# Performance work log

Hardware: AMD Instinct MI355X
Metric: run time of the kernel (lower is better)

Reference implementation:

```python
import jax, jax.numpy as jnp
import numpy as np

B, S, H = 4, 4096, 256
NH, W = 8, 128
DH = H // NH
FF = 1024
NEG = -1e9

def gelu(x):
    return jax.nn.gelu(x, approximate=False)

def layer_norm(x, g, b, eps=1e-9):
    # torch .std() is unbiased (ddof=1); note the (std + eps) denominator, not sqrt(var+eps)
    mean = jnp.mean(x, axis=-1, keepdims=True)
    std = jnp.std(x, axis=-1, keepdims=True, ddof=1)
    return g * (x - mean) / (std + eps) + b

def causal_conv(x, w, b, dilation):
    # x: (B,S,C), w: (9, Cin, Cout); left-padded causal conv (Conv class)
    pad = dilation * 8
    y = jax.lax.conv_general_dilated(x, w, window_strides=(1,), padding=[(pad, 0)],
                                     rhs_dilation=(dilation,), dimension_numbers=('NWC', 'WIO', 'NWC'))
    return y + b

def sliding_window_attention(q, k, v, bias):
    # q,k,v: (B,NH,S,DH); q pre-scaled. Faithful to Longformer sliding_chunks_matmul_qk/pv:
    # band of 2W+1 relative offsets per query, out-of-range keys masked to -inf before softmax.
    b, h, s, d = q.shape
    c = s // W  # number of length-W query chunks
    qc = q.reshape(b, h, c, W, d)
    kp = jnp.pad(k, ((0, 0), (0, 0), (W, W), (0, 0)))
    vp = jnp.pad(v, ((0, 0), (0, 0), (W, W), (0, 0)))
    kidx = (jnp.arange(c) * W)[:, None] + jnp.arange(3 * W)[None, :]  # (c,3W) overlapping key chunks
    kc = kp[:, :, kidx, :]  # (b,h,c,3W,d)
    vc = vp[:, :, kidx, :]
    scores = jnp.einsum('bhcxd,bhcyd->bhcxy', qc, kc)  # (b,h,c,W,3W)
    x = jnp.arange(W)
    r = jnp.arange(2 * W + 1)
    band_idx = x[:, None] + r[None, :]  # (W,2W+1), values in [0,3W-1]
    band = jnp.take_along_axis(scores, band_idx[None, None, None], axis=-1)  # (b,h,c,W,2W+1)
    i = jnp.arange(s).reshape(c, W)
    j = i[:, :, None] + (r - W)[None, None, :]  # global key index per band entry
    valid = (j >= 0) & (j < s)
    band = jnp.where(valid[None, None], band + bias, NEG)  # relative bias depends only on offset
    probs = jax.nn.softmax(band.astype(jnp.float32), axis=-1).astype(q.dtype)
    ridx = jnp.arange(3 * W)[None, :] - x[:, None]  # (W,3W) inverse band->chunk map
    vmask = ((ridx >= 0) & (ridx <= 2 * W)).astype(probs.dtype)
    pc = jnp.take_along_axis(probs, jnp.clip(ridx, 0, 2 * W)[None, None, None], axis=-1) * vmask[None, None, None]
    return jnp.einsum('bhcxy,bhcyd->bhcxd', pc, vc).reshape(b, h, s, d)


def setup_inputs() -> dict:
    key = jax.random.key(0)
    ks = jax.random.split(key, 12)
    inputs = jax.random.normal(ks[0], (B, S, H), jnp.float32)
    dw_w = jax.random.normal(ks[1], (9,), jnp.float32) * 0.1   # depthwise (9,1) kernel, 1 channel
    dw_b = jnp.zeros((1,), jnp.float32)
    pw_w = jax.random.normal(ks[2], (3,), jnp.float32) * 0.5   # pointwise 1->3 conv (scalars)
    pw_b = jnp.zeros((3,), jnp.float32)
    Wq = jax.random.normal(ks[3], (H, H), jnp.float32) * 0.02
    Wk = jax.random.normal(ks[4], (H, H), jnp.float32) * 0.02
    Wv = jax.random.normal(ks[5], (H, H), jnp.float32) * 0.02
    Wo = jax.random.normal(ks[6], (H, H), jnp.float32) * 0.02
    rel_bias = jax.random.normal(ks[7], (2 * S,), jnp.float32) * 0.02
    ln1_g = jnp.ones((H,), jnp.float32); ln1_b = jnp.zeros((H,), jnp.float32)
    ln2_g = jnp.ones((H,), jnp.float32); ln2_b = jnp.zeros((H,), jnp.float32)
    w1 = jax.random.normal(ks[8], (9, H, FF), jnp.float32) * 0.02
    b1 = jnp.zeros((FF,), jnp.float32)
    w2 = jax.random.normal(ks[9], (9, FF, H), jnp.float32) * 0.02
    b2 = jnp.zeros((H,), jnp.float32)
    return {"inputs": inputs, "dw_w": dw_w, "dw_b": dw_b, "pw_w": pw_w, "pw_b": pw_b,
            "Wq": Wq, "Wk": Wk, "Wv": Wv, "Wo": Wo, "rel_bias": rel_bias,
            "ln1_g": ln1_g, "ln1_b": ln1_b, "ln2_g": ln2_g, "ln2_b": ln2_b,
            "w1": w1, "b1": b1, "w2": w2, "b2": b2}


def reference(inputs, dw_w, dw_b, pw_w, pw_b, Wq, Wk, Wv, Wo, rel_bias,
              ln1_g, ln1_b, ln2_g, ln2_b, w1, b1, w2, b2):
    x = inputs
    xn = layer_norm(x, ln1_g, ln1_b)
    # SepConv2d QKV generator: depthwise (9,1) conv along seq (shared over features), GELU,
    # pointwise 1x1 conv 1->3 channels, then GELU again (self.relu in MHA.forward)
    xp = jnp.pad(xn, ((0, 0), (4, 4), (0, 0)))
    dw = jnp.zeros_like(xn)
    for t in range(9):
        dw = dw + dw_w[t] * xp[:, t:t + S, :]
    dw = dw + dw_b[0]
    hmid = gelu(dw)
    qkv = gelu(hmid[None] * pw_w.reshape(3, 1, 1, 1) + pw_b.reshape(3, 1, 1, 1))  # (3,B,S,H)
    q = qkv[0] @ Wq
    k = qkv[1] @ Wk
    v = qkv[2] @ Wv
    split = lambda t: t.reshape(B, S, NH, DH).transpose(0, 2, 1, 3)
    q, k, v = split(q), split(k), split(v)
    q = q * (DH ** -0.5)
    # relative_position_index = arange(2W+1).repeat(lens,1) -> bias uses table[:2W+1] per offset
    bias = rel_bias[:2 * W + 1]
    ctx = sliding_window_attention(q, k, v, bias)
    ctx = ctx.transpose(0, 2, 1, 3).reshape(B, S, H)
    x = x + ctx @ Wo
    xn2 = layer_norm(x, ln2_g, ln2_b)
    # PositionwiseFeedForward 'cc': causal dilated convs; GELU applied after every layer (incl. last)
    f = gelu(causal_conv(xn2, w1, b1, 1))
    f = gelu(causal_conv(f, w2, b2, 8))
    return x + f
```

## Files before the change

### kernel.cpp

```cpp
#include <hip/hip_runtime.h>
#include <stdint.h>

typedef uint16_t u16;
typedef uint32_t u32;

typedef __attribute__((ext_vector_type(8))) short bf16x8;
typedef __attribute__((ext_vector_type(4))) float f32x4;

typedef __attribute__((address_space(1))) const u32 gas_u32;
typedef __attribute__((address_space(3))) u32 las_u32;

#define S_LEN 4096
#define HDIM  256
#define FFDIM 1024

__device__ __forceinline__ float bf2f(u16 u) { return __uint_as_float(((u32)u) << 16); }
__device__ __forceinline__ u16 f2bf(float f) {
  u32 x = __float_as_uint(f);
  return (u16)((x + 0x7fffu + ((x >> 16) & 1u)) >> 16);
}
__device__ __forceinline__ float gelu_f(float x) {
  return 0.5f * x * (1.0f + erff(x * 0.7071067811865475f));
}
__device__ __forceinline__ void glds16(const u16* g, u16* l) {
  __builtin_amdgcn_global_load_lds((gas_u32*)g, (las_u32*)l, 16, 0, 0);
}

__global__ __launch_bounds__(256) void ktranspose_all(
    const float* __restrict__ Wq, const float* __restrict__ Wk, const float* __restrict__ Wv,
    const float* __restrict__ Wo, const float* __restrict__ W1, const float* __restrict__ W2,
    u16* __restrict__ WqT, u16* __restrict__ WkT, u16* __restrict__ WvT,
    u16* __restrict__ WoT, u16* __restrict__ W1T, u16* __restrict__ W2T, float qscale) {
  __shared__ u16 t[32][33];
  const int bid = blockIdx.x;
  const float* in; u16* out; int K, N; float scale = 1.0f; int idx;
  if (bid < 256) {
    K = 256; N = 256; idx = bid & 63;
    const int w = bid >> 6;
    in = (w == 0) ? Wq : (w == 1) ? Wk : (w == 2) ? Wv : Wo;
    out = (w == 0) ? WqT : (w == 1) ? WkT : (w == 2) ? WvT : WoT;
    if (w == 0) scale = qscale;
  } else if (bid < 2560) {
    K = 2304; N = 1024; idx = bid - 256; in = W1; out = W1T;
  } else {
    K = 9216; N = 256; idx = bid - 2560; in = W2; out = W2T;
  }
  const int kt = K >> 5;
  const int k0 = (idx % kt) * 32, n0 = (idx / kt) * 32;
  const int tx = threadIdx.x, ty = threadIdx.y;
#pragma unroll
  for (int i = ty; i < 32; i += 8) t[i][tx] = f2bf(in[(long)(k0 + i) * N + (n0 + tx)] * scale);
  __syncthreads();
#pragma unroll
  for (int i = ty; i < 32; i += 8) out[(long)(n0 + i) * K + (k0 + tx)] = t[tx][i];
}

template <int OUTBF>
__global__ __launch_bounds__(256) void ln_kernel(const float* __restrict__ inv, void* __restrict__ outv,
                                                 const float* __restrict__ g, const float* __restrict__ bsh,
                                                 int OSEGR, int OGUARD,
                                                 uint4* __restrict__ gx, uint4* __restrict__ gf) {
  const int tid = threadIdx.x;
  if (OUTBF && blockIdx.x >= 4096) {
    int t = (blockIdx.x - 4096) * 256 + tid;
    const uint4 z = {0u, 0u, 0u, 0u};
    if (t < 1024) {
      const int s = t >> 8, o = t & 255;
      gx[(long)s * 131328 + o] = z;
    } else {
      t -= 1024;
      if (t < 32768) {
        const int s = t >> 13, o = t & 8191;
        gf[(long)s * 532480 + o] = z;
      }
    }
    return;
  }
  const int lane = tid & 63;
  const long row = (long)blockIdx.x * 4 + (tid >> 6);
  const int c0 = lane * 4;
  float v[4];
  float4 f = *(const float4*)(inv + row * HDIM + c0);
  v[0] = f.x; v[1] = f.y; v[2] = f.z; v[3] = f.w;
  float s = v[0] + v[1] + v[2] + v[3];
#pragma unroll
  for (int o = 32; o > 0; o >>= 1) s += __shfl_xor(s, o);
  const float mean = s * (1.0f / 256.0f);
  float ss = 0.f;
#pragma unroll
  for (int j = 0; j < 4; ++j) { float d = v[j] - mean; ss += d * d; }
#pragma unroll
  for (int o = 32; o > 0; o >>= 1) ss += __shfl_xor(ss, o);
  const float inv_ = 1.0f / (sqrtf(ss * (1.0f / 255.0f)) + 1e-9f);
  float y[4];
#pragma unroll
  for (int j = 0; j < 4; ++j) y[j] = g[c0 + j] * (v[j] - mean) * inv_ + bsh[c0 + j];
  if (OUTBF) {
    const long orow = (row >> 12) * OSEGR + OGUARD + (row & (S_LEN - 1));
    uint2 o_;
    o_.x = (u32)f2bf(y[0]) | ((u32)f2bf(y[1]) << 16);
    o_.y = (u32)f2bf(y[2]) | ((u32)f2bf(y[3]) << 16);
    *(uint2*)((u16*)outv + orow * HDIM + c0) = o_;
  } else {
    float4 o_; o_.x = y[0]; o_.y = y[1]; o_.z = y[2]; o_.w = y[3];
    *(float4*)((float*)outv + row * HDIM + c0) = o_;
  }
}

__global__ __launch_bounds__(256) void dwconv_qkv(const float* __restrict__ xn,
                                                  u16* __restrict__ gq, u16* __restrict__ gk, u16* __restrict__ gv,
                                                  const float* __restrict__ dw_w, const float* __restrict__ dw_b,
                                                  const float* __restrict__ pw_w, const float* __restrict__ pw_b) {
  const int tid = threadIdx.x;
  const int lane = tid & 63;
  const long row = (long)blockIdx.x * 4 + (tid >> 6);
  const int sl = (int)(row & (S_LEN - 1));
  const float b0 = dw_b[0];
  float a0 = b0, a1 = b0, a2 = b0, a3 = b0;
#pragma unroll
  for (int t = 0; t < 9; ++t) {
    const int s2 = sl + t - 4;
    if (s2 >= 0 && s2 < S_LEN) {
      const float w = dw_w[t];
      float4 xv = *(const float4*)(xn + (row + t - 4) * HDIM + lane * 4);
      a0 = fmaf(w, xv.x, a0); a1 = fmaf(w, xv.y, a1);
      a2 = fmaf(w, xv.z, a2); a3 = fmaf(w, xv.w, a3);
    }
  }
  float h[4];
  h[0] = gelu_f(a0); h[1] = gelu_f(a1); h[2] = gelu_f(a2); h[3] = gelu_f(a3);
  u16* outs[3] = {gq, gk, gv};
#pragma unroll
  for (int p = 0; p < 3; ++p) {
    const float pw = pw_w[p], pb = pw_b[p];
    float y[4];
#pragma unroll
    for (int j = 0; j < 4; ++j) y[j] = gelu_f(fmaf(h[j], pw, pb));
    uint2 o_;
    o_.x = (u32)f2bf(y[0]) | ((u32)f2bf(y[1]) << 16);
    o_.y = (u32)f2bf(y[2]) | ((u32)f2bf(y[3]) << 16);
    *(uint2*)(outs[p] + row * HDIM + lane * 4) = o_;
  }
}

__global__ __launch_bounds__(256) void gemm_big(
    const u16* __restrict__ A, const u16* __restrict__ BT, void* __restrict__ Outv,
    u16* __restrict__ vt, int KW, int N, long a_z, long b_z, long o_z) {
  __shared__ __align__(16) u16 As[256 * 64];
  __shared__ __align__(16) u16 Bs[128 * 64];
  const int tid = threadIdx.x;
  const int lane = tid & 63;
  const int wid = tid >> 6;
  const int wm = (wid & 1) * 128;
  const int wn = (wid >> 1) * 64;
  const int fm = lane & 15;
  const int fq = lane >> 4;
  const int t0 = blockIdx.x * 256;
  const int n0 = blockIdx.y * 128;
  A += (long)blockIdx.z * a_z;
  BT += (long)blockIdx.z * b_z;

  const int srow = lane >> 3;
  const int cseg = (((lane & 7) ^ srow) << 3);

  f32x4 acc[8][4];
#pragma unroll
  for (int a = 0; a < 8; ++a)
#pragma unroll
    for (int b = 0; b < 4; ++b) acc[a][b] = (f32x4){0.f, 0.f, 0.f, 0.f};

  for (int k0 = 0; k0 < KW; k0 += 64) {
    for (int op = wid; op < 32; op += 4)
      glds16(A + (long)(t0 + op * 8 + srow) * KW + k0 + cseg, &As[op * 8 * 64]);
#pragma unroll
    for (int j = 0; j < 4; ++j)
      glds16(BT + (long)(n0 + wid * 32 + j * 8 + srow) * KW + k0 + cseg,
             &Bs[(wid * 32 + j * 8) * 64]);
    __syncthreads();
#pragma unroll
    for (int kk = 0; kk < 2; ++kk) {
      const int g = kk * 4 + fq;
      bf16x8 af[8], bfv[4];
#pragma unroll
      for (int t = 0; t < 8; ++t) {
        const int ra = wm + t * 16 + fm;
        af[t] = *(const bf16x8*)&As[ra * 64 + ((g ^ (ra & 7)) << 3)];
      }
#pragma unroll
      for (int t = 0; t < 4; ++t) {
        const int rb = wn + t * 16 + fm;
        bfv[t] = *(const bf16x8*)&Bs[rb * 64 + ((g ^ (rb & 7)) << 3)];
      }
#pragma unroll
      for (int mi = 0; mi < 8; ++mi)
#pragma unroll
        for (int ni = 0; ni < 4; ++ni)
          acc[mi][ni] = __builtin_amdgcn_mfma_f32_16x16x32_bf16(af[mi], bfv[ni], acc[mi][ni], 0, 0, 0);
    }
    __syncthreads();
  }

#pragma unroll
  for (int mi = 0; mi < 8; ++mi)
#pragma unroll
    for (int ni = 0; ni < 4; ++ni) {
      if (blockIdx.z == 2) {
        const int col = n0 + wn + ni * 16 + fm;
        const int hh = col >> 5, dd = col & 31;
        const long trow0 = t0 + wm + mi * 16 + fq * 4;
        const long bb = trow0 >> 12;
        const int s0 = (int)(trow0 & (S_LEN - 1));
        uint2 o_;
        o_.x = (u32)f2bf(acc[mi][ni][0]) | ((u32)f2bf(acc[mi][ni][1]) << 16);
        o_.y = (u32)f2bf(acc[mi][ni][2]) | ((u32)f2bf(acc[mi][ni][3]) << 16);
        *(uint2*)(vt + ((bb * 8 + hh) * 32 + dd) * S_LEN + s0) = o_;
      } else {
#pragma unroll
        for (int r = 0; r < 4; ++r) {
          const long trow = t0 + wm + mi * 16 + fq * 4 + r;
          const int col = n0 + wn + ni * 16 + fm;
          ((u16*)Outv + (long)blockIdx.z * o_z)[trow * N + col] = f2bf(acc[mi][ni][r]);
        }
      }
    }
}

__global__ __launch_bounds__(256) void gemm_wo(
    const u16* __restrict__ A, const u16* __restrict__ BT, float* __restrict__ Outv,
    const float* __restrict__ residv, int KW, int N) {
  __shared__ __align__(16) u16 As[128 * 64];
  __shared__ __align__(16) u16 Bs[128 * 64];
  const int tid = threadIdx.x;
  const int lane = tid & 63;
  const int wid = tid >> 6;
  const int wm = (wid & 1) * 64;
  const int wn = (wid >> 1) * 64;
  const int fm = lane & 15;
  const int fq = lane >> 4;
  const int t0 = blockIdx.x * 128;
  const int n0 = blockIdx.y * 128;

  const int srow = lane >> 3;
  const int cseg = (((lane & 7) ^ srow) << 3);

  f32x4 acc[4][4];
#pragma unroll
  for (int a = 0; a < 4; ++a)
#pragma unroll
    for (int b = 0; b < 4; ++b) acc[a][b] = (f32x4){0.f, 0.f, 0.f, 0.f};

  u16* alb = &As[wid * 32 * 64];
  u16* blb = &Bs[wid * 32 * 64];

  for (int k0 = 0; k0 < KW; k0 += 64) {
    const u16* ag = A + (long)(t0 + wid * 32 + srow) * KW + k0 + cseg;
    const u16* bg = BT + (long)(n0 + wid * 32 + srow) * KW + k0 + cseg;
#pragma unroll
    for (int j = 0; j < 4; ++j) {
      glds16(ag + (long)(8 * j) * KW, alb + j * 8 * 64);
      glds16(bg + (long)(8 * j) * KW, blb + j * 8 * 64);
    }
    __syncthreads();
#pragma unroll
    for (int kk = 0; kk < 2; ++kk) {
      const int g = kk * 4 + fq;
      bf16x8 af[4], bfv[4];
#pragma unroll
      for (int t = 0; t < 4; ++t) {
        const int ra = wm + t * 16 + fm;
        af[t] = *(const bf16x8*)&As[ra * 64 + ((g ^ (ra & 7)) << 3)];
        const int rb = wn + t * 16 + fm;
        bfv[t] = *(const bf16x8*)&Bs[rb * 64 + ((g ^ (rb & 7)) << 3)];
      }
#pragma unroll
      for (int mi = 0; mi < 4; ++mi)
#pragma unroll
        for (int ni = 0; ni < 4; ++ni)
          acc[mi][ni] = __builtin_amdgcn_mfma_f32_16x16x32_bf16(af[mi], bfv[ni], acc[mi][ni], 0, 0, 0);
    }
    __syncthreads();
  }

#pragma unroll
  for (int mi = 0; mi < 4; ++mi)
#pragma unroll
    for (int ni = 0; ni < 4; ++ni)
#pragma unroll
      for (int r = 0; r < 4; ++r) {
        const long trow = t0 + wm + mi * 16 + fq * 4 + r;
        const int col = n0 + wn + ni * 16 + fm;
        Outv[trow * N + col] = acc[mi][ni][r] + residv[trow * N + col];
      }
}

__global__ __launch_bounds__(256) void attn_mfma(const u16* __restrict__ Q, const u16* __restrict__ K,
                                                 const u16* __restrict__ VT, const float* __restrict__ rel,
                                                 u16* __restrict__ CTX) {
  __shared__ __align__(16) u16 Ks[384 * 36];
  __shared__ __align__(16) u16 VTs[32 * 388];
  __shared__ __align__(16) u16 Ps[4][32 * 72];
  __shared__ float bias_s[260];
  const int c = blockIdx.x, h = blockIdx.y, b = blockIdx.z;
  const int tid = threadIdx.x;
  const int lane = tid & 63, wid = tid >> 6;
  const int fm = lane & 15, fq = lane >> 4;
  const int j0 = c * 128 - 128;
  const long kvbase = ((long)b * S_LEN) * HDIM + h * 32;
  const long vtbase = (((long)b * 8 + h) * 32) * S_LEN;

  for (int idx = tid; idx < 384 * 4; idx += 256) {
    const int jj = idx >> 2, seg = (idx & 3) * 8;
    int j = j0 + jj; j = j < 0 ? 0 : (j > S_LEN - 1 ? S_LEN - 1 : j);
    uint4 kv = *(const uint4*)(K + kvbase + (long)j * HDIM + seg);
    *(uint4*)&Ks[jj * 36 + seg] = kv;
  }
#pragma unroll
  for (int p = 0; p < 6; ++p) {
    const int idx = p * 256 + tid;
    const int d = idx / 48, seg = idx - d * 48;
    int off = j0 + seg * 8; off = off < 0 ? 0 : (off > S_LEN - 8 ? S_LEN - 8 : off);
    uint4 vv = *(const uint4*)(VT + vtbase + (long)d * S_LEN + off);
    *(uint4*)&VTs[d * 388 + seg * 8] = vv;
  }
  for (int idx = tid; idx < 257; idx += 256) bias_s[idx] = rel[idx];
  __syncthreads();

  bf16x8 aq[2];
#pragma unroll
  for (int mi = 0; mi < 2; ++mi)
    aq[mi] = *(const bf16x8*)(Q + kvbase + (long)(c * 128 + wid * 32 + mi * 16 + fm) * HDIM + fq * 8);

  const int klo = (c == 0) ? 128 : 0;
  const int khi = (c == 31) ? 255 : 383;

  float m_r[2][4], l_r[2][4];
  f32x4 acc[2][2];
#pragma unroll
  for (int mi = 0; mi < 2; ++mi)
#pragma unroll
    for (int r = 0; r < 4; ++r) { m_r[mi][r] = -1e9f; l_r[mi][r] = 0.f; }
#pragma unroll
  for (int mi = 0; mi < 2; ++mi)
#pragma unroll
    for (int nd = 0; nd < 2; ++nd) acc[mi][nd] = (f32x4){0.f, 0.f, 0.f, 0.f};

  u16* pw = &Ps[wid][0];

  for (int ch = 0; ch < 6; ++ch) {
    f32x4 sc[2][4];
#pragma unroll
    for (int ni = 0; ni < 4; ++ni) {
      bf16x8 bk = *(const bf16x8*)&Ks[(ch * 64 + ni * 16 + fm) * 36 + fq * 8];
#pragma unroll
      for (int mi = 0; mi < 2; ++mi)
        sc[mi][ni] = __builtin_amdgcn_mfma_f32_16x16x32_bf16(aq[mi], bk, (f32x4){0.f, 0.f, 0.f, 0.f}, 0, 0, 0);
    }
    float cm[2][4];
#pragma unroll
    for (int mi = 0; mi < 2; ++mi)
#pragma unroll
      for (int r = 0; r < 4; ++r) cm[mi][r] = -1e9f;
#pragma unroll
    for (int mi = 0; mi < 2; ++mi)
#pragma unroll
      for (int ni = 0; ni < 4; ++ni) {
        const int keyloc = ch * 64 + ni * 16 + fm;
        const bool kval = (keyloc >= klo) && (keyloc <= khi);
#pragma unroll
        for (int r = 0; r < 4; ++r) {
          const int qloc = wid * 32 + mi * 16 + fq * 4 + r;
          const int rr = keyloc - qloc;
          const bool valid = kval && (rr >= 0) && (rr <= 256);
          const int rc = valid ? rr : 0;
          float vv = sc[mi][ni][r] + bias_s[rc];
          vv = valid ? vv : -1e9f;
          sc[mi][ni][r] = vv;
          cm[mi][r] = fmaxf(cm[mi][r], vv);
        }
      }
#pragma unroll
    for (int mi = 0; mi < 2; ++mi)
#pragma unroll
      for (int r = 0; r < 4; ++r) {
        float x = cm[mi][r];
        x = fmaxf(x, __shfl_xor(x, 1));
        x = fmaxf(x, __shfl_xor(x, 2));
        x = fmaxf(x, __shfl_xor(x, 4));
        x = fmaxf(x, __shfl_xor(x, 8));
        cm[mi][r] = x;
      }
    float alpha[2][4];
#pragma unroll
    for (int mi = 0; mi < 2; ++mi)
#pragma unroll
      for (int r = 0; r < 4; ++r) {
        const float nm = fmaxf(m_r[mi][r], cm[mi][r]);
        alpha[mi][r] = __expf(m_r[mi][r] - nm);
        m_r[mi][r] = nm;
        l_r[mi][r] *= alpha[mi][r];
      }
#pragma unroll
    for (int mi = 0; mi < 2; ++mi)
#pragma unroll
      for (int nd = 0; nd < 2; ++nd)
#pragma unroll
        for (int r = 0; r < 4; ++r) acc[mi][nd][r] *= alpha[mi][r];
#pragma unroll
    for (int mi = 0; mi < 2; ++mi)
#pragma unroll
      for (int ni = 0; ni < 4; ++ni)
#pragma unroll
        for (int r = 0; r < 4; ++r) {
          const float pv = __expf(sc[mi][ni][r] - m_r[mi][r]);
          l_r[mi][r] += pv;
          pw[(mi * 16 + fq * 4 + r) * 72 + ni * 16 + fm] = f2bf(pv);
        }
#pragma unroll
    for (int kc = 0; kc < 2; ++kc) {
      bf16x8 ap[2], bv[2];
#pragma unroll
      for (int mi = 0; mi < 2; ++mi)
        ap[mi] = *(const bf16x8*)&pw[(mi * 16 + fm) * 72 + kc * 32 + fq * 8];
#pragma unroll
      for (int nd = 0; nd < 2; ++nd)
        bv[nd] = *(const bf16x8*)&VTs[(nd * 16 + fm) * 388 + ch * 64 + kc * 32 + fq * 8];
#pragma unroll
      for (int mi = 0; mi < 2; ++mi)
#pragma unroll
        for (int nd = 0; nd < 2; ++nd)
          acc[mi][nd] = __builtin_amdgcn_mfma_f32_16x16x32_bf16(ap[mi], bv[nd], acc[mi][nd], 0, 0, 0);
    }
  }

  float linv[2][4];
#pragma unroll
  for (int mi = 0; mi < 2; ++mi)
#pragma unroll
    for (int r = 0; r < 4; ++r) {
      float x = l_r[mi][r];
      x += __shfl_xor(x, 1);
      x += __shfl_xor(x, 2);
      x += __shfl_xor(x, 4);
      x += __shfl_xor(x, 8);
      linv[mi][r] = 1.0f / x;
    }
#pragma unroll
  for (int mi = 0; mi < 2; ++mi)
#pragma unroll
    for (int nd = 0; nd < 2; ++nd)
#pragma unroll
      for (int r = 0; r < 4; ++r) {
        const long s = c * 128 + wid * 32 + mi * 16 + fq * 4 + r;
        CTX[((long)b * S_LEN + s) * HDIM + h * 32 + nd * 16 + fm] = f2bf(acc[mi][nd][r] * linv[mi][r]);
      }
}

template <int APITCH, int NTAPS, int DIL, int NN>
__global__ __launch_bounds__(256, 2) void gemm_conv(
    const u16* __restrict__ Apad, const u16* __restrict__ BT, void* __restrict__ Outv,
    const float* __restrict__ bias,
    int SEGR, int BPITCH, int OSEGR, int OGUARD) {
  constexpr int AROWS = 256 + (NTAPS - 1) * DIL;
  constexpr int AOPS = (AROWS + 7) / 8;
  __shared__ __align__(16) u16 As[AOPS * 8 * 64];
  __shared__ __align__(16) u16 Bs2[2][128 * 64];
  const int tid = threadIdx.x;
  const int lane = tid & 63;
  const int wid = tid >> 6;
  const int wm = (wid & 1) * 128;
  const int wn = (wid >> 1) * 64;
  const int fm = lane & 15;
  const int fq = lane >> 4;
  const int t0 = blockIdx.x * 256;
  const int n0 = blockIdx.y * 128;

  const int seg = t0 >> 12;
  const long abase = (long)seg * SEGR + (t0 & (S_LEN - 1));
  const int srow = lane >> 3;
  const int cseg = (((lane & 7) ^ srow) << 3);

  f32x4 acc[8][4];
#pragma unroll
  for (int a = 0; a < 8; ++a)
#pragma unroll
    for (int b = 0; b < 4; ++b) acc[a][b] = (f32x4){0.f, 0.f, 0.f, 0.f};

  for (int k0 = 0; k0 < APITCH; k0 += 64) {
    for (int op = wid; op < AOPS; op += 4)
      glds16(Apad + (abase + op * 8 + srow) * APITCH + k0 + cseg, &As[op * 8 * 64]);
#pragma unroll
    for (int j = 0; j < 4; ++j)
      glds16(BT + (long)(n0 + wid * 32 + j * 8 + srow) * BPITCH + k0 + cseg,
             &Bs2[0][(wid * 32 + j * 8) * 64]);
    __syncthreads();
#pragma unroll
    for (int u = 0; u < NTAPS; ++u) {
      if (u + 1 < NTAPS) {
        const long bc = (long)(u + 1) * APITCH + k0;
#pragma unroll
        for (int j = 0; j < 4; ++j)
          glds16(BT + (long)(n0 + wid * 32 + j * 8 + srow) * BPITCH + bc + cseg,
                 &Bs2[(u + 1) & 1][(wid * 32 + j * 8) * 64]);
      }
      const int du = u * DIL;
      const u16* bsp = Bs2[u & 1];
#pragma unroll
      for (int kk = 0; kk < 2; ++kk) {
        const int g = kk * 4 + fq;
        bf16x8 af[8], bfv[4];
#pragma unroll
        for (int t = 0; t < 8; ++t) {
          const int ra = wm + t * 16 + fm + du;
          af[t] = *(const bf16x8*)&As[ra * 64 + ((g ^ (ra & 7)) << 3)];
        }
#pragma unroll
        for (int t = 0; t < 4; ++t) {
          const int rb = wn + t * 16 + fm;
          bfv[t] = *(const bf16x8*)&bsp[rb * 64 + ((g ^ (rb & 7)) << 3)];
        }
#pragma unroll
        for (int mi = 0; mi < 8; ++mi)
#pragma unroll
          for (int ni = 0; ni < 4; ++ni)
            acc[mi][ni] = __builtin_amdgcn_mfma_f32_16x16x32_bf16(af[mi], bfv[ni], acc[mi][ni], 0, 0, 0);
      }
      __syncthreads();
    }
  }

#pragma unroll
  for (int mi = 0; mi < 8; ++mi)
#pragma unroll
    for (int ni = 0; ni < 4; ++ni)
#pragma unroll
      for (int r = 0; r < 4; ++r) {
        const long trow = t0 + wm + mi * 16 + fq * 4 + r;
        const int col = n0 + wn + ni * 16 + fm;
        const long orow = (trow >> 12) * OSEGR + OGUARD + (trow & (S_LEN - 1));
        ((u16*)Outv)[orow * NN + col] = f2bf(gelu_f(acc[mi][ni][r] + bias[col]));
      }
}

__global__ __launch_bounds__(256) void gemm_conv_s(
    const u16* __restrict__ Apad, const u16* __restrict__ BT, float* __restrict__ Outv,
    int APITCH, int SEGR, int BPITCH, int ntaps, int dil, int N, long out_z_off) {
  __shared__ __align__(16) u16 As[144 * 64];
  __shared__ __align__(16) u16 Bs2[2][128 * 64];
  const int tid = threadIdx.x;
  const int lane = tid & 63;
  const int wid = tid >> 6;
  const int wm = (wid & 1) * 64;
  const int wn = (wid >> 1) * 64;
  const int fm = lane & 15;
  const int fq = lane >> 4;
  const int t0 = blockIdx.x * 128;
  const int n0 = blockIdx.y * 128;
  const int tap0 = blockIdx.z * ntaps;

  const int seg = t0 >> 12;
  const long abase = (long)seg * SEGR + (t0 & (S_LEN - 1)) + (long)tap0 * dil;
  const int aops = (128 + (ntaps - 1) * dil + 7) >> 3;

  const int srow = lane >> 3;
  const int cseg = (((lane & 7) ^ srow) << 3);

  f32x4 acc[4][4];
#pragma unroll
  for (int a = 0; a < 4; ++a)
#pragma unroll
    for (int b = 0; b < 4; ++b) acc[a][b] = (f32x4){0.f, 0.f, 0.f, 0.f};

  for (int k0 = 0; k0 < APITCH; k0 += 64) {
    for (int op = wid; op < aops; op += 4)
      glds16(Apad + (abase + op * 8 + srow) * APITCH + k0 + cseg, &As[op * 8 * 64]);
    {
      const long bc = (long)tap0 * APITCH + k0;
#pragma unroll
      for (int j = 0; j < 4; ++j)
        glds16(BT + (long)(n0 + wid * 32 + j * 8 + srow) * BPITCH + bc + cseg,
               &Bs2[0][(wid * 32 + j * 8) * 64]);
    }
    __syncthreads();
    for (int u = 0; u < ntaps; ++u) {
      if (u + 1 < ntaps) {
        const long bc = (long)(tap0 + u + 1) * APITCH + k0;
#pragma unroll
        for (int j = 0; j < 4; ++j)
          glds16(BT + (long)(n0 + wid * 32 + j * 8 + srow) * BPITCH + bc + cseg,
                 &Bs2[(u + 1) & 1][(wid * 32 + j * 8) * 64]);
      }
      const int du = u * dil;
      const u16* bsp = Bs2[u & 1];
#pragma unroll
      for (int kk = 0; kk < 2; ++kk) {
        const int g = kk * 4 + fq;
        bf16x8 af[4], bfv[4];
#pragma unroll
        for (int t = 0; t < 4; ++t) {
          const int ra = wm + t * 16 + fm + du;
          af[t] = *(const bf16x8*)&As[ra * 64 + ((g ^ (ra & 7)) << 3)];
          const int rb = wn + t * 16 + fm;
          bfv[t] = *(const bf16x8*)&bsp[rb * 64 + ((g ^ (rb & 7)) << 3)];
        }
#pragma unroll
        for (int mi = 0; mi < 4; ++mi)
#pragma unroll
          for (int ni = 0; ni < 4; ++ni)
            acc[mi][ni] = __builtin_amdgcn_mfma_f32_16x16x32_bf16(af[mi], bfv[ni], acc[mi][ni], 0, 0, 0);
      }
      __syncthreads();
    }
  }

#pragma unroll
  for (int mi = 0; mi < 4; ++mi)
#pragma unroll
    for (int ni = 0; ni < 4; ++ni)
#pragma unroll
      for (int r = 0; r < 4; ++r) {
        const long trow = t0 + wm + mi * 16 + fq * 4 + r;
        const int col = n0 + wn + ni * 16 + fm;
        (Outv + (long)blockIdx.z * out_z_off)[trow * N + col] = acc[mi][ni][r];
      }
}

__global__ __launch_bounds__(256) void final_kernel(const float* __restrict__ x2, const float* __restrict__ P,
                                                    const float* __restrict__ b2, float* __restrict__ out) {
  const long i4 = ((long)blockIdx.x * 256 + threadIdx.x) * 4;
  const int c0 = (int)(i4 & (HDIM - 1));
  float4 xa = *(const float4*)(x2 + i4);
  float4 p0 = *(const float4*)(P + i4);
  float4 p1 = *(const float4*)(P + 4194304 + i4);
  float4 p2 = *(const float4*)(P + 8388608 + i4);
  const float pv[4] = {p0.x + p1.x + p2.x, p0.y + p1.y + p2.y, p0.z + p1.z + p2.z, p0.w + p1.w + p2.w};
  float4 o_;
  o_.x = xa.x + gelu_f(pv[0] + b2[c0 + 0]);
  o_.y = xa.y + gelu_f(pv[1] + b2[c0 + 1]);
  o_.z = xa.z + gelu_f(pv[2] + b2[c0 + 2]);
  o_.w = xa.w + gelu_f(pv[3] + b2[c0 + 3]);
  *(float4*)(out + i4) = o_;
}

extern "C" void kernel_launch(void* const* d_in, const int* in_sizes, int n_in,
                              void* d_out, int out_size, void* d_ws, size_t ws_size,
                              hipStream_t stream) {
  (void)in_sizes; (void)n_in; (void)out_size;
  const float* X    = (const float*)d_in[0];
  const float* dw_w = (const float*)d_in[1];
  const float* dw_b = (const float*)d_in[2];
  const float* pw_w = (const float*)d_in[3];
  const float* pw_b = (const float*)d_in[4];
  const float* Wq   = (const float*)d_in[5];
  const float* Wk   = (const float*)d_in[6];
  const float* Wv   = (const float*)d_in[7];
  const float* Wo   = (const float*)d_in[8];
  const float* rel  = (const float*)d_in[9];
  const float* ln1g = (const float*)d_in[10];
  const float* ln1b = (const float*)d_in[11];
  const float* ln2g = (const float*)d_in[12];
  const float* ln2b = (const float*)d_in[13];
  const float* w1   = (const float*)d_in[14];
  const float* b1   = (const float*)d_in[15];
  const float* w2   = (const float*)d_in[16];
  const float* b2   = (const float*)d_in[17];

  if (ws_size < 119537664) return;

  char* ws = (char*)d_ws;
  u16* WqT = (u16*)(ws + 0);
  u16* WkT = (u16*)(ws + 131072);
  u16* WvT = (u16*)(ws + 262144);
  u16* WoT = (u16*)(ws + 393216);
  u16* W1T = (u16*)(ws + 524288);
  u16* W2T = (u16*)(ws + 5242880);
  float* xn  = (float*)(ws + 10485760);
  float* x2  = xn;
  u16* gq  = (u16*)(ws + 27262976);
  u16* gk  = (u16*)(ws + 35651584);
  u16* gv  = (u16*)(ws + 44040192);
  u16* q   = (u16*)(ws + 52428800);
  u16* vt  = (u16*)(ws + 69206016);
  u16* ctx = (u16*)(ws + 77594624);
  u16* f1p  = (u16*)(ws + 27262976);
  u16* xn2p = (u16*)(ws + 61341696);
  float* P  = (float*)(ws + 61341696);

  const float qscale = 0.17677669529663687f;
  ktranspose_all<<<4864, dim3(32, 8), 0, stream>>>(Wq, Wk, Wv, Wo, w1, w2,
      WqT, WkT, WvT, WoT, W1T, W2T, qscale);

  ln_kernel<0><<<4096, 256, 0, stream>>>(X, xn, ln1g, ln1b, 4096, 0, nullptr, nullptr);
  dwconv_qkv<<<4096, 256, 0, stream>>>(xn, gq, gk, gv, dw_w, dw_b, pw_w, pw_b);

  gemm_big<<<dim3(64, 2, 3), 256, 0, stream>>>(gq, WqT, q, vt,
      256, 256, 4194304, 65536, 4194304);

  attn_mfma<<<dim3(32, 8, 4), 256, 0, stream>>>(q, q + 4194304, vt, rel, ctx);

  gemm_wo<<<dim3(128, 2), 256, 0, stream>>>(ctx, WoT, x2, X, 256, 256);

  ln_kernel<1><<<4228, 256, 0, stream>>>(x2, xn2p, ln2g, ln2b, 4104, 8,
      (uint4*)xn2p, (uint4*)f1p);

  gemm_conv<256, 9, 1, 1024><<<dim3(64, 8), 256, 0, stream>>>(
      xn2p, W1T, f1p, b1, 4104, 2304, 4160, 64);

  gemm_conv_s<<<dim3(128, 2, 3), 256, 0, stream>>>(f1p, W2T, P,
      1024, 4160, 9216, 3, 8, 256, 4194304);

  final_kernel<<<4096, 256, 0, stream>>>(x2, P, b2, (float*)d_out);
}
```

Baseline: 389.2 us.

## Fuse weight transpose, LN1 and depthwise QKV into one kernel; store split-K partials as bf16

The weight transpose, first layer norm and depthwise-conv/GELU QKV generation now run as one launch. Extra blocks recompute LN1 for a 16-row tile plus a 4-row halo into shared memory, so the fp32 normalized activations no longer round-trip through global memory. The split-K partial outputs of the second FFN conv GEMM are stored as bf16 instead of fp32, which halves that write and the final reduction's read but loses precision in the partial sums. The first FFN conv GEMM grid is flattened so adjacent blocks share an A tile across N.

```diff
diff --git a/kernel.cpp b/kernel.cpp
--- a/kernel.cpp
+++ b/kernel.cpp
@@ -26,42 +26,110 @@
   __builtin_amdgcn_global_load_lds((gas_u32*)g, (las_u32*)l, 16, 0, 0);
 }
 
-__global__ __launch_bounds__(256) void ktranspose_all(
+__global__ __launch_bounds__(256) void front_kernel(
     const float* __restrict__ Wq, const float* __restrict__ Wk, const float* __restrict__ Wv,
     const float* __restrict__ Wo, const float* __restrict__ W1, const float* __restrict__ W2,
     u16* __restrict__ WqT, u16* __restrict__ WkT, u16* __restrict__ WvT,
-    u16* __restrict__ WoT, u16* __restrict__ W1T, u16* __restrict__ W2T, float qscale) {
+    u16* __restrict__ WoT, u16* __restrict__ W1T, u16* __restrict__ W2T, float qscale,
+    const float* __restrict__ X, u16* __restrict__ gq, u16* __restrict__ gk, u16* __restrict__ gv,
+    const float* __restrict__ ln1g, const float* __restrict__ ln1b,
+    const float* __restrict__ dw_w, const float* __restrict__ dw_b,
+    const float* __restrict__ pw_w, const float* __restrict__ pw_b) {
   __shared__ u16 t[32][33];
+  __shared__ float xnl[24 * 256];
   const int bid = blockIdx.x;
-  const float* in; u16* out; int K, N; float scale = 1.0f; int idx;
-  if (bid < 256) {
-    K = 256; N = 256; idx = bid & 63;
-    const int w = bid >> 6;
-    in = (w == 0) ? Wq : (w == 1) ? Wk : (w == 2) ? Wv : Wo;
-    out = (w == 0) ? WqT : (w == 1) ? WkT : (w == 2) ? WvT : WoT;
-    if (w == 0) scale = qscale;
-  } else if (bid < 2560) {
-    K = 2304; N = 1024; idx = bid - 256; in = W1; out = W1T;
-  } else {
-    K = 9216; N = 256; idx = bid - 2560; in = W2; out = W2T;
-  }
-  const int kt = K >> 5;
-  const int k0 = (idx % kt) * 32, n0 = (idx / kt) * 32;
-  const int tx = threadIdx.x, ty = threadIdx.y;
-#pragma unroll
-  for (int i = ty; i < 32; i += 8) t[i][tx] = f2bf(in[(long)(k0 + i) * N + (n0 + tx)] * scale);
+  const int tid = threadIdx.x;
+  if (bid < 4864) {
+    const float* in; u16* out; int K, N; float scale = 1.0f; int idx;
+    if (bid < 256) {
+      K = 256; N = 256; idx = bid & 63;
+      const int w = bid >> 6;
+      in = (w == 0) ? Wq : (w == 1) ? Wk : (w == 2) ? Wv : Wo;
+      out = (w == 0) ? WqT : (w == 1) ? WkT : (w == 2) ? WvT : WoT;
+      if (w == 0) scale = qscale;
+    } else if (bid < 2560) {
+      K = 2304; N = 1024; idx = bid - 256; in = W1; out = W1T;
+    } else {
+      K = 9216; N = 256; idx = bid - 2560; in = W2; out = W2T;
+    }
+    const int kt = K >> 5;
+    const int k0 = (idx % kt) * 32, n0 = (idx / kt) * 32;
+    const int tx = tid & 31, ty = tid >> 5;
+#pragma unroll
+    for (int i = ty; i < 32; i += 8) t[i][tx] = f2bf(in[(long)(k0 + i) * N + (n0 + tx)] * scale);
+    __syncthreads();
+#pragma unroll
+    for (int i = ty; i < 32; i += 8) out[(long)(n0 + i) * K + (k0 + tx)] = t[tx][i];
+    return;
+  }
+  const int ro = (bid - 4864) * 16;
+  const int seg_lo = ro & ~(S_LEN - 1);
+  const int lane = tid & 63;
+  const int ri = tid >> 6;
+  const int c0 = lane * 4;
+#pragma unroll
+  for (int p = 0; p < 6; ++p) {
+    const int h = ro - 4 + p * 4 + ri;
+    float y[4] = {0.f, 0.f, 0.f, 0.f};
+    if (h >= seg_lo && h < seg_lo + S_LEN) {
+      float4 f = *(const float4*)(X + (long)h * HDIM + c0);
+      float v[4] = {f.x, f.y, f.z, f.w};
+      float s = v[0] + v[1] + v[2] + v[3];
+#pragma unroll
+      for (int o = 32; o > 0; o >>= 1) s += __shfl_xor(s, o);
+      const float mean = s * (1.0f / 256.0f);
+      float ss = 0.f;
+#pragma unroll
+      for (int j = 0; j < 4; ++j) { float d = v[j] - mean; ss += d * d; }
+#pragma unroll
+      for (int o = 32; o > 0; o >>= 1) ss += __shfl_xor(ss, o);
+      const float inv_ = 1.0f / (sqrtf(ss * (1.0f / 255.0f)) + 1e-9f);
+#pragma unroll
+      for (int j = 0; j < 4; ++j) y[j] = ln1g[c0 + j] * (v[j] - mean) * inv_ + ln1b[c0 + j];
+    }
+    float4 o_; o_.x = y[0]; o_.y = y[1]; o_.z = y[2]; o_.w = y[3];
+    *(float4*)&xnl[(p * 4 + ri) * 256 + c0] = o_;
+  }
   __syncthreads();
-#pragma unroll
-  for (int i = ty; i < 32; i += 8) out[(long)(n0 + i) * K + (k0 + tx)] = t[tx][i];
-}
-
-template <int OUTBF>
-__global__ __launch_bounds__(256) void ln_kernel(const float* __restrict__ inv, void* __restrict__ outv,
-                                                 const float* __restrict__ g, const float* __restrict__ bsh,
-                                                 int OSEGR, int OGUARD,
-                                                 uint4* __restrict__ gx, uint4* __restrict__ gf) {
+  const float b0 = dw_b[0];
+  float wv[9];
+#pragma unroll
+  for (int q = 0; q < 9; ++q) wv[q] = dw_w[q];
+  const float pwv[3] = {pw_w[0], pw_w[1], pw_w[2]};
+  const float pbv[3] = {pw_b[0], pw_b[1], pw_b[2]};
+  u16* outs[3] = {gq, gk, gv};
+#pragma unroll
+  for (int p = 0; p < 4; ++p) {
+    const int lrow = p * 4 + ri;
+    float a0 = b0, a1 = b0, a2 = b0, a3 = b0;
+#pragma unroll
+    for (int q = 0; q < 9; ++q) {
+      const float w = wv[q];
+      float4 xv = *(const float4*)&xnl[(lrow + q) * 256 + c0];
+      a0 = fmaf(w, xv.x, a0); a1 = fmaf(w, xv.y, a1);
+      a2 = fmaf(w, xv.z, a2); a3 = fmaf(w, xv.w, a3);
+    }
+    float h[4];
+    h[0] = gelu_f(a0); h[1] = gelu_f(a1); h[2] = gelu_f(a2); h[3] = gelu_f(a3);
+    const long orow = (long)(ro + lrow);
+#pragma unroll
+    for (int pp = 0; pp < 3; ++pp) {
+      float y[4];
+#pragma unroll
+      for (int j = 0; j < 4; ++j) y[j] = gelu_f(fmaf(h[j], pwv[pp], pbv[pp]));
+      uint2 o_;
+      o_.x = (u32)f2bf(y[0]) | ((u32)f2bf(y[1]) << 16);
+      o_.y = (u32)f2bf(y[2]) | ((u32)f2bf(y[3]) << 16);
+      *(uint2*)(outs[pp] + orow * HDIM + c0) = o_;
+    }
+  }
+}
+
+__global__ __launch_bounds__(256) void ln2_kernel(const float* __restrict__ inv, u16* __restrict__ outv,
+                                                  const float* __restrict__ g, const float* __restrict__ bsh,
+                                                  uint4* __restrict__ gx, uint4* __restrict__ gf) {
   const int tid = threadIdx.x;
-  if (OUTBF && blockIdx.x >= 4096) {
+  if (blockIdx.x >= 4096) {
     int t = (blockIdx.x - 4096) * 256 + tid;
     const uint4 z = {0u, 0u, 0u, 0u};
     if (t < 1024) {
@@ -95,52 +163,11 @@
   float y[4];
 #pragma unroll
   for (int j = 0; j < 4; ++j) y[j] = g[c0 + j] * (v[j] - mean) * inv_ + bsh[c0 + j];
-  if (OUTBF) {
-    const long orow = (row >> 12) * OSEGR + OGUARD + (row & (S_LEN - 1));
-    uint2 o_;
-    o_.x = (u32)f2bf(y[0]) | ((u32)f2bf(y[1]) << 16);
-    o_.y = (u32)f2bf(y[2]) | ((u32)f2bf(y[3]) << 16);
-    *(uint2*)((u16*)outv + orow * HDIM + c0) = o_;
-  } else {
-    float4 o_; o_.x = y[0]; o_.y = y[1]; o_.z = y[2]; o_.w = y[3];
-    *(float4*)((float*)outv + row * HDIM + c0) = o_;
-  }
-}
-
-__global__ __launch_bounds__(256) void dwconv_qkv(const float* __restrict__ xn,
-                                                  u16* __restrict__ gq, u16* __restrict__ gk, u16* __restrict__ gv,
-                                                  const float* __restrict__ dw_w, const float* __restrict__ dw_b,
-                                                  const float* __restrict__ pw_w, const float* __restrict__ pw_b) {
-  const int tid = threadIdx.x;
-  const int lane = tid & 63;
-  const long row = (long)blockIdx.x * 4 + (tid >> 6);
-  const int sl = (int)(row & (S_LEN - 1));
-  const float b0 = dw_b[0];
-  float a0 = b0, a1 = b0, a2 = b0, a3 = b0;
-#pragma unroll
-  for (int t = 0; t < 9; ++t) {
-    const int s2 = sl + t - 4;
-    if (s2 >= 0 && s2 < S_LEN) {
-      const float w = dw_w[t];
-      float4 xv = *(const float4*)(xn + (row + t - 4) * HDIM + lane * 4);
-      a0 = fmaf(w, xv.x, a0); a1 = fmaf(w, xv.y, a1);
-      a2 = fmaf(w, xv.z, a2); a3 = fmaf(w, xv.w, a3);
-    }
-  }
-  float h[4];
-  h[0] = gelu_f(a0); h[1] = gelu_f(a1); h[2] = gelu_f(a2); h[3] = gelu_f(a3);
-  u16* outs[3] = {gq, gk, gv};
-#pragma unroll
-  for (int p = 0; p < 3; ++p) {
-    const float pw = pw_w[p], pb = pw_b[p];
-    float y[4];
-#pragma unroll
-    for (int j = 0; j < 4; ++j) y[j] = gelu_f(fmaf(h[j], pw, pb));
-    uint2 o_;
-    o_.x = (u32)f2bf(y[0]) | ((u32)f2bf(y[1]) << 16);
-    o_.y = (u32)f2bf(y[2]) | ((u32)f2bf(y[3]) << 16);
-    *(uint2*)(outs[p] + row * HDIM + lane * 4) = o_;
-  }
+  const long orow = (row >> 12) * 4104 + 8 + (row & (S_LEN - 1));
+  uint2 o_;
+  o_.x = (u32)f2bf(y[0]) | ((u32)f2bf(y[1]) << 16);
+  o_.y = (u32)f2bf(y[2]) | ((u32)f2bf(y[3]) << 16);
+  *(uint2*)(outv + orow * HDIM + c0) = o_;
 }
 
 __global__ __launch_bounds__(256) void gemm_big(
@@ -471,8 +498,8 @@
   const int wn = (wid >> 1) * 64;
   const int fm = lane & 15;
   const int fq = lane >> 4;
-  const int t0 = blockIdx.x * 256;
-  const int n0 = blockIdx.y * 128;
+  const int t0 = (blockIdx.x >> 3) * 256;
+  const int n0 = (blockIdx.x & 7) * 128;
 
   const int seg = t0 >> 12;
   const long abase = (long)seg * SEGR + (t0 & (S_LEN - 1));
@@ -542,7 +569,7 @@
 }
 
 __global__ __launch_bounds__(256) void gemm_conv_s(
-    const u16* __restrict__ Apad, const u16* __restrict__ BT, float* __restrict__ Outv,
+    const u16* __restrict__ Apad, const u16* __restrict__ BT, u16* __restrict__ Outv,
     int APITCH, int SEGR, int BPITCH, int ntaps, int dil, int N, long out_z_off) {
   __shared__ __align__(16) u16 As[144 * 64];
   __shared__ __align__(16) u16 Bs2[2][128 * 64];
@@ -620,19 +647,23 @@
       for (int r = 0; r < 4; ++r) {
         const long trow = t0 + wm + mi * 16 + fq * 4 + r;
         const int col = n0 + wn + ni * 16 + fm;
-        (Outv + (long)blockIdx.z * out_z_off)[trow * N + col] = acc[mi][ni][r];
-      }
-}
-
-__global__ __launch_bounds__(256) void final_kernel(const float* __restrict__ x2, const float* __restrict__ P,
+        (Outv + (long)blockIdx.z * out_z_off)[trow * N + col] = f2bf(acc[mi][ni][r]);
+      }
+}
+
+__global__ __launch_bounds__(256) void final_kernel(const float* __restrict__ x2, const u16* __restrict__ P,
                                                     const float* __restrict__ b2, float* __restrict__ out) {
   const long i4 = ((long)blockIdx.x * 256 + threadIdx.x) * 4;
   const int c0 = (int)(i4 & (HDIM - 1));
   float4 xa = *(const float4*)(x2 + i4);
-  float4 p0 = *(const float4*)(P + i4);
-  float4 p1 = *(const float4*)(P + 4194304 + i4);
-  float4 p2 = *(const float4*)(P + 8388608 + i4);
-  const float pv[4] = {p0.x + p1.x + p2.x, p0.y + p1.y + p2.y, p0.z + p1.z + p2.z, p0.w + p1.w + p2.w};
+  uint2 u0 = *(const uint2*)(P + i4);
+  uint2 u1 = *(const uint2*)(P + 4194304 + i4);
+  uint2 u2 = *(const uint2*)(P + 8388608 + i4);
+  float pv[4];
+  pv[0] = bf2f((u16)(u0.x & 0xffffu)) + bf2f((u16)(u1.x & 0xffffu)) + bf2f((u16)(u2.x & 0xffffu));
+  pv[1] = bf2f((u16)(u0.x >> 16)) + bf2f((u16)(u1.x >> 16)) + bf2f((u16)(u2.x >> 16));
+  pv[2] = bf2f((u16)(u0.y & 0xffffu)) + bf2f((u16)(u1.y & 0xffffu)) + bf2f((u16)(u2.y & 0xffffu));
+  pv[3] = bf2f((u16)(u0.y >> 16)) + bf2f((u16)(u1.y >> 16)) + bf2f((u16)(u2.y >> 16));
   float4 o_;
   o_.x = xa.x + gelu_f(pv[0] + b2[c0 + 0]);
   o_.y = xa.y + gelu_f(pv[1] + b2[c0 + 1]);
@@ -673,8 +704,7 @@
   u16* WoT = (u16*)(ws + 393216);
   u16* W1T = (u16*)(ws + 524288);
   u16* W2T = (u16*)(ws + 5242880);
-  float* xn  = (float*)(ws + 10485760);
-  float* x2  = xn;
+  float* x2  = (float*)(ws + 10485760);
   u16* gq  = (u16*)(ws + 27262976);
   u16* gk  = (u16*)(ws + 35651584);
   u16* gv  = (u16*)(ws + 44040192);
@@ -683,14 +713,12 @@
   u16* ctx = (u16*)(ws + 77594624);
   u16* f1p  = (u16*)(ws + 27262976);
   u16* xn2p = (u16*)(ws + 61341696);
-  float* P  = (float*)(ws + 61341696);
+  u16* P    = (u16*)(ws + 61341696);
 
   const float qscale = 0.17677669529663687f;
-  ktranspose_all<<<4864, dim3(32, 8), 0, stream>>>(Wq, Wk, Wv, Wo, w1, w2,
-      WqT, WkT, WvT, WoT, W1T, W2T, qscale);
-
-  ln_kernel<0><<<4096, 256, 0, stream>>>(X, xn, ln1g, ln1b, 4096, 0, nullptr, nullptr);
-  dwconv_qkv<<<4096, 256, 0, stream>>>(xn, gq, gk, gv, dw_w, dw_b, pw_w, pw_b);
+  front_kernel<<<5888, 256, 0, stream>>>(Wq, Wk, Wv, Wo, w1, w2,
+      WqT, WkT, WvT, WoT, W1T, W2T, qscale,
+      X, gq, gk, gv, ln1g, ln1b, dw_w, dw_b, pw_w, pw_b);
 
   gemm_big<<<dim3(64, 2, 3), 256, 0, stream>>>(gq, WqT, q, vt,
       256, 256, 4194304, 65536, 4194304);
@@ -699,10 +727,9 @@
 
   gemm_wo<<<dim3(128, 2), 256, 0, stream>>>(ctx, WoT, x2, X, 256, 256);
 
-  ln_kernel<1><<<4228, 256, 0, stream>>>(x2, xn2p, ln2g, ln2b, 4104, 8,
-      (uint4*)xn2p, (uint4*)f1p);
-
-  gemm_conv<256, 9, 1, 1024><<<dim3(64, 8), 256, 0, stream>>>(
+  ln2_kernel<<<4228, 256, 0, stream>>>(x2, xn2p, ln2g, ln2b, (uint4*)xn2p, (uint4*)f1p);
+
+  gemm_conv<256, 9, 1, 1024><<<512, 256, 0, stream>>>(
       xn2p, W1T, f1p, b1, 4104, 2304, 4160, 64);
 
   gemm_conv_s<<<dim3(128, 2, 3), 256, 0, stream>>>(f1p, W2T, P,
```

Result: faster. 380.9 us (-2.1%).
